# Optimization experiments

Measured on AMD Instinct MI355X. Metric: run time of the kernel, lower is better.

Reference implementation:

```python
import jax, jax.numpy as jnp
import numpy as np

DX = 1.0
DZ_MIN = 1.0
K = 3  # median filter kernel size (odd)


def median_filter3d(x):
    # x: (N, C, D, H, W); 3x3x3 windowed median with reflect padding.
    p = K // 2
    xp = jnp.pad(x, ((0, 0), (0, 0), (p, p), (p, p), (p, p)), mode='reflect')
    N, C, D, H, W = x.shape
    # 27 shifted views stacked on a new last axis (fixed small loop over kernel offsets)
    wins = jnp.stack(
        [xp[:, :, i:i + D, j:j + H, k:k + W]
         for i in range(K) for j in range(K) for k in range(K)],
        axis=-1,
    )
    # 27 elements (odd) -> torch lower-median == element at index 13 of sorted window
    return jnp.sort(wins, axis=-1)[..., (K * K * K - 1) // 2]


def setup_inputs() -> dict:
    key = jax.random.key(0)
    pred_z = jax.random.normal(key, (1, 1, 128, 192, 193), dtype=jnp.float32)
    return {"pred_z": pred_z, "iepoch": 1, "epoch_max": 100}


def reference(pred_z, iepoch, epoch_max):
    # dz along last (W) axis
    dz = pred_z[..., 1:] - pred_z[..., :-1]
    d = dz / DX
    # windowed-median smoothness loss (no NaNs in inputs -> nanmean == mean)
    smoothz = median_filter3d(d)
    loss_smooth = jnp.mean((d - smoothz) ** 2)
    # monotonicity penalty: max over clamped negative increments
    loss_mon = jnp.max(jnp.maximum(-(dz - DZ_MIN) / DX, 0.0))
    # torch.median over all elements returns sorted[(n-1)//2] (lower median)
    z0 = pred_z[..., 0].reshape(-1)
    n = z0.shape[0]
    loss_average = jnp.sort(z0)[(n - 1) // 2] ** 2
    return (loss_smooth, loss_mon, loss_average)
```

## Files before the change

### kernel.cpp

```cpp
#include <hip/hip_runtime.h>

#define NZ 128
#define NY 192
#define NXP 193
#define NX 192
#define NVOX (NZ * NY * NX)
#define NZ0 (NZ * NY)

#define TX 32
#define TY 16
#define TZ 8
#define LX 34
#define LY 18
#define LZ 10
#define LSL (LY * LX)
#define LTOT (LZ * LSL)

#define GX (NX / TX)
#define GY (NY / TY)
#define GZ (NZ / TZ)
#define NBLK (GX * GY * GZ)
#define ZB (NZ0 / 256)

__device__ double   g_ps[NBLK];
__device__ float    g_pm[NBLK];
__device__ unsigned g_hist[2048];
__device__ unsigned g_u[NZ0];

__device__ __forceinline__ int refl(int i, int n) {
    i = (i < 0) ? -i : i;
    i = (i >= n) ? (2 * n - 2 - i) : i;
    return i;
}

__device__ __forceinline__ unsigned f2sortable(float f) {
    unsigned bits = __float_as_uint(f);
    return bits ^ ((bits & 0x80000000u) ? 0xFFFFFFFFu : 0x80000000u);
}

template<int M, int N>
struct OEM {
    static __device__ __forceinline__ void run(const float* a, const float* b, float* out) {
        if constexpr (M == 0) {
#pragma unroll
            for (int i = 0; i < N; ++i) out[i] = b[i];
        } else if constexpr (N == 0) {
#pragma unroll
            for (int i = 0; i < M; ++i) out[i] = a[i];
        } else if constexpr (M == 1 && N == 1) {
            out[0] = fminf(a[0], b[0]);
            out[1] = fmaxf(a[0], b[0]);
        } else {
            constexpr int ME = (M + 1) / 2, MO = M / 2, NE = (N + 1) / 2, NO = N / 2;
            float ae[ME], be[NE];
            float ao[MO > 0 ? MO : 1], bo[NO > 0 ? NO : 1];
#pragma unroll
            for (int i = 0; i < ME; ++i) ae[i] = a[2 * i];
#pragma unroll
            for (int i = 0; i < MO; ++i) ao[i] = a[2 * i + 1];
#pragma unroll
            for (int i = 0; i < NE; ++i) be[i] = b[2 * i];
#pragma unroll
            for (int i = 0; i < NO; ++i) bo[i] = b[2 * i + 1];
            constexpr int EL = ME + NE, OL = MO + NO;
            float e[EL];
            float o[OL > 0 ? OL : 1];
            OEM<ME, NE>::run(ae, be, e);
            OEM<MO, NO>::run(ao, bo, o);
            constexpr int P = (OL < EL - 1) ? OL : (EL - 1);
            out[0] = e[0];
#pragma unroll
            for (int i = 0; i < P; ++i) {
                out[2 * i + 1] = fminf(o[i], e[i + 1]);
                out[2 * i + 2] = fmaxf(o[i], e[i + 1]);
            }
            if constexpr (EL == OL)           out[M + N - 1] = o[OL - 1];
            else if constexpr (EL == OL + 2)  out[M + N - 1] = e[EL - 1];
        }
    }
};

template<int N>
struct OES {
    static __device__ __forceinline__ void run(const float* in, float* out) {
        if constexpr (N == 1) {
            out[0] = in[0];
        } else {
            constexpr int H = N / 2;
            float s1[H], s2[N - H];
            OES<H>::run(in, s1);
            OES<N - H>::run(in + H, s2);
            OEM<H, N - H>::run(s1, s2, out);
        }
    }
};

__device__ __forceinline__ float sel27(const float* A, const float* M) {
    float t0 = fmaxf(A[0], M[12]);
    float t1 = fmaxf(A[1], M[11]);
    float t2 = fmaxf(A[2], M[10]);
    float t3 = fmaxf(A[3], M[9]);
    float t4 = fmaxf(A[4], M[8]);
    float t5 = fmaxf(A[5], M[7]);
    float t6 = fmaxf(A[6], M[6]);
    float t7 = fmaxf(A[7], M[5]);
    float t8 = fmaxf(A[8], M[4]);
    float r0 = fminf(fminf(t0, t1), fminf(t2, t3));
    float r1 = fminf(fminf(t4, t5), fminf(t6, t7));
    return fminf(fminf(r0, r1), fminf(t8, M[13]));
}

__global__ __launch_bounds__(256, 3) void fused_main(const float* __restrict__ P) {
    __shared__ float dt[LTOT];
    const int tid = threadIdx.x;
    const int bid = blockIdx.x;

    if (bid < ZB) {
        unsigned* h = (unsigned*)dt;
        for (int j = tid; j < 2048; j += 256) h[j] = 0u;
        __syncthreads();
        const int i = bid * 256 + tid;
        unsigned u = f2sortable(P[(size_t)i * NXP]);
        g_u[i] = u;
        atomicAdd(&h[u >> 21], 1u);
        __syncthreads();
        for (int j = tid; j < 2048; j += 256) {
            unsigned c = h[j];
            if (c) atomicAdd(&g_hist[j], c);
        }
        return;
    }

    const int bf = bid - ZB;
    const int bx = bf % GX;
    const int brem = bf / GX;
    const int by = brem % GY;
    const int bz = brem / GY;
    const int x0 = bx * TX, y0 = by * TY, z0t = bz * TZ;

    int goff[3], lp[3];
#pragma unroll
    for (int k = 0; k < 3; ++k) {
        int p = tid + 256 * k;
        lp[k] = (p < LSL) ? p : -1;
        if (p < LSL) {
            int xx = p % LX, yy = p / LX;
            int gy = refl(y0 + yy - 1, NY);
            int gx = refl(x0 + xx - 1, NX);
            goff[k] = gy * NXP + gx;
        }
    }
    for (int zz = 0; zz < LZ; ++zz) {
        int gz = refl(z0t + zz - 1, NZ);
        const float* __restrict__ pl = P + (size_t)gz * (NY * NXP);
#pragma unroll
        for (int k = 0; k < 3; ++k) {
            if (lp[k] >= 0) {
                float a = pl[goff[k]];
                float b = pl[goff[k] + 1];
                dt[zz * LSL + lp[k]] = b - a;
            }
        }
    }
    __syncthreads();

    const int x = tid & 31;
    const int y = tid >> 5;
    const int lbA = y * LX + x;
    const int lbB = lbA + 8 * LX;

    auto rd9 = [&](int base, float* v) {
#pragma unroll
        for (int dy = 0; dy < 3; ++dy)
#pragma unroll
            for (int dxx = 0; dxx < 3; ++dxx)
                v[dy * 3 + dxx] = dt[base + dy * LX + dxx];
    };

    float SA0[9], SA1[9], SA2[9], SB0[9], SB1[9], SB2[9];
    float cA, cB, s_acc = 0.0f, m_acc = 0.0f;

    {
        float a9[9], b9[9];
        rd9(lbA, a9);            rd9(lbB, b9);
        OES<9>::run(a9, SA0);    OES<9>::run(b9, SB0);
        rd9(lbA + LSL, a9);      rd9(lbB + LSL, b9);
        cA = a9[4];              cB = b9[4];
        OES<9>::run(a9, SA1);    OES<9>::run(b9, SB1);
    }

    auto pairstep = [&](float (&XA)[9], float (&YA)[9], float (&ZA)[9],
                        float (&XB)[9], float (&YB)[9], float (&ZB_)[9], int t) {
        float a9[9], b9[9], MA[18], MB[18];
        rd9(lbA + (t + 2) * LSL, a9);
        rd9(lbB + (t + 2) * LSL, b9);
        float cnA = a9[4], cnB = b9[4];
        OES<9>::run(a9, ZA);            OES<9>::run(b9, ZB_);
        OEM<9, 9>::run(YA, ZA, MA);     OEM<9, 9>::run(YB, ZB_, MB);
        float medA = sel27(XA, MA), medB = sel27(XB, MB);
        float dA = cA - medA, dB = cB - medB;
        s_acc = fmaf(dA, dA, fmaf(dB, dB, s_acc));
        m_acc = fmaxf(m_acc, fmaxf(1.0f - cA, 1.0f - cB));
        cA = cnA; cB = cnB;
        rd9(lbA + (t + 3) * LSL, a9);
        rd9(lbB + (t + 3) * LSL, b9);
        cnA = a9[4]; cnB = b9[4];
        OES<9>::run(a9, XA);            OES<9>::run(b9, XB);
        medA = sel27(XA, MA);           medB = sel27(XB, MB);
        dA = cA - medA; dB = cB - medB;
        s_acc = fmaf(dA, dA, fmaf(dB, dB, s_acc));
        m_acc = fmaxf(m_acc, fmaxf(1.0f - cA, 1.0f - cB));
        cA = cnA; cB = cnB;
    };

    pairstep(SA0, SA1, SA2, SB0, SB1, SB2, 0);
    pairstep(SA2, SA0, SA1, SB2, SB0, SB1, 2);
    pairstep(SA1, SA2, SA0, SB1, SB2, SB0, 4);
    pairstep(SA0, SA1, SA2, SB0, SB1, SB2, 6);

#pragma unroll
    for (int off = 32; off > 0; off >>= 1) {
        s_acc += __shfl_down(s_acc, off);
        m_acc = fmaxf(m_acc, __shfl_down(m_acc, off));
    }
    __shared__ float ss[4], sm[4];
    const int lane = tid & 63, wid = tid >> 6;
    if (lane == 0) { ss[wid] = s_acc; sm[wid] = m_acc; }
    __syncthreads();
    if (tid == 0) {
        float S = (ss[0] + ss[1]) + (ss[2] + ss[3]);
        float M = fmaxf(fmaxf(sm[0], sm[1]), fmaxf(sm[2], sm[3]));
        g_ps[bf] = (double)S;
        g_pm[bf] = M;
    }
}

__global__ __launch_bounds__(1024) void final_k(float* __restrict__ out) {
    __shared__ unsigned cand[2048];
    __shared__ unsigned s_cnt, s_med, s_b, s_r;
    __shared__ unsigned wsum[16], woff[16];
    const int tid = threadIdx.x;
    const int lane = tid & 63, wid = tid >> 6;
    const unsigned kk = (NZ0 - 1) / 2;

    unsigned h0 = g_hist[2 * tid], h1 = g_hist[2 * tid + 1];
    {
        unsigned mysum = h0 + h1, inc = mysum;
#pragma unroll
        for (int d = 1; d < 64; d <<= 1) { unsigned t2 = __shfl_up(inc, d); if (lane >= d) inc += t2; }
        if (lane == 63) wsum[wid] = inc;
        __syncthreads();
        if (tid == 0) { unsigned a = 0; for (int w = 0; w < 16; ++w) { woff[w] = a; a += wsum[w]; } }
        __syncthreads();
        unsigned exc = woff[wid] + inc - mysum;
        if (exc <= kk && kk < exc + h0) { s_b = 2u * tid; s_r = kk - exc; }
        exc += h0;
        if (exc <= kk && kk < exc + h1) { s_b = 2u * tid + 1u; s_r = kk - exc; }
    }
    __syncthreads();
    const unsigned b1 = s_b, k1 = s_r;
    g_hist[2 * tid] = 0u; g_hist[2 * tid + 1] = 0u;

    if (tid == 0) s_cnt = 0u;
    __syncthreads();
    for (int i = tid; i < NZ0; i += 1024) {
        unsigned u = g_u[i];
        if ((u >> 21) == b1) {
            unsigned idx = atomicAdd(&s_cnt, 1u);
            if (idx < 2048u) cand[idx] = u;
        }
    }
    __syncthreads();
    const unsigned m = s_cnt;

    if (m <= 2048u) {
        for (int i = tid; i < (int)m; i += 1024) {
            unsigned c = cand[i], less = 0u, eq = 0u;
            for (unsigned j = 0; j < m; ++j) {
                unsigned v = cand[j];
                less += (v < c); eq += (v == c);
            }
            if (less <= k1 && k1 < less + eq) s_med = c;
        }
        __syncthreads();
    } else {
        unsigned pref = b1, kx = k1;
        for (int j = tid; j < 2048; j += 1024) cand[j] = 0u;
        __syncthreads();
        for (int i = tid; i < NZ0; i += 1024) {
            unsigned u = g_u[i];
            if ((u >> 21) == pref) atomicAdd(&cand[(u >> 10) & 2047u], 1u);
        }
        __syncthreads();
        {
            unsigned c0 = cand[tid * 2], c1 = cand[tid * 2 + 1];
            unsigned mysum = c0 + c1, inc = mysum;
#pragma unroll
            for (int d = 1; d < 64; d <<= 1) { unsigned t2 = __shfl_up(inc, d); if (lane >= d) inc += t2; }
            if (lane == 63) wsum[wid] = inc;
            __syncthreads();
            if (tid == 0) { unsigned a = 0; for (int w = 0; w < 16; ++w) { woff[w] = a; a += wsum[w]; } }
            __syncthreads();
            unsigned exc = woff[wid] + inc - mysum;
            if (exc <= kx && kx < exc + c0) { s_b = tid * 2u; s_r = kx - exc; }
            exc += c0;
            if (exc <= kx && kx < exc + c1) { s_b = tid * 2u + 1u; s_r = kx - exc; }
        }
        __syncthreads();
        pref = (pref << 11) | s_b; kx = s_r;
        __syncthreads();
        for (int j = tid; j < 1024; j += 1024) cand[j] = 0u;
        __syncthreads();
        for (int i = tid; i < NZ0; i += 1024) {
            unsigned u = g_u[i];
            if ((u >> 10) == pref) atomicAdd(&cand[u & 1023u], 1u);
        }
        __syncthreads();
        {
            unsigned c0 = cand[tid], mysum = c0, inc = mysum;
#pragma unroll
            for (int d = 1; d < 64; d <<= 1) { unsigned t2 = __shfl_up(inc, d); if (lane >= d) inc += t2; }
            if (lane == 63) wsum[wid] = inc;
            __syncthreads();
            if (tid == 0) { unsigned a = 0; for (int w = 0; w < 16; ++w) { woff[w] = a; a += wsum[w]; } }
            __syncthreads();
            unsigned exc = woff[wid] + inc - mysum;
            if (exc <= kx && kx < exc + c0) s_b = (unsigned)tid;
        }
        __syncthreads();
        if (tid == 0) s_med = (pref << 10) | s_b;
        __syncthreads();
    }

    double s = 0.0; float mm = 0.0f;
    if (tid < NBLK) { s = g_ps[tid]; mm = g_pm[tid]; }
    if (tid < NBLK - 1024) { s += g_ps[1024 + tid]; mm = fmaxf(mm, g_pm[1024 + tid]); }
#pragma unroll
    for (int off = 32; off > 0; off >>= 1) {
        s += __shfl_down(s, off);
        mm = fmaxf(mm, __shfl_down(mm, off));
    }
    __shared__ double sd[16];
    __shared__ float sf[16];
    if (lane == 0) { sd[wid] = s; sf[wid] = mm; }
    __syncthreads();
    if (tid == 0) {
        double S = 0.0; float M = 0.0f;
        for (int w = 0; w < 16; ++w) { S += sd[w]; M = fmaxf(M, sf[w]); }
        unsigned u = s_med;
        unsigned bits = (u & 0x80000000u) ? (u ^ 0x80000000u) : ~u;
        float med = __uint_as_float(bits);
        out[0] = (float)(S / (double)NVOX);
        out[1] = M;
        out[2] = med * med;
    }
}

extern "C" void kernel_launch(void* const* d_in, const int* in_sizes, int n_in,
                              void* d_out, int out_size, void* d_ws, size_t ws_size,
                              hipStream_t stream) {
    const float* P = (const float*)d_in[0];
    float* out = (float*)d_out;

    hipLaunchKernelGGL(fused_main, dim3(ZB + NBLK), dim3(256), 0, stream, P);
    hipLaunchKernelGGL(final_k, dim3(1), dim3(1024), 0, stream, out);
}
```

Measured before the change: 104.5 us.

## Fuse final reduction into main kernel via last-block ticket

Merges the separate single-block final kernel into the main kernel. Each block takes an atomic ticket after a threadfence, and the last block to finish does the histogram median selection and the partial-sum reduction with 256 threads. This removes the second kernel launch and the gap between kernels. In exchange the tail work runs on 256 threads instead of 1024, and there is an extra atomic plus a fence in every block.

```diff
diff --git a/kernel.cpp b/kernel.cpp
--- a/kernel.cpp
+++ b/kernel.cpp
@@ -21,11 +21,13 @@
 #define GZ (NZ / TZ)
 #define NBLK (GX * GY * GZ)
 #define ZB (NZ0 / 256)
+#define NBALL (ZB + NBLK)
 
 __device__ double   g_ps[NBLK];
 __device__ float    g_pm[NBLK];
 __device__ unsigned g_hist[2048];
 __device__ unsigned g_u[NZ0];
+__device__ unsigned g_ticket;
 
 __device__ __forceinline__ int refl(int i, int n) {
     i = (i < 0) ? -i : i;
@@ -110,10 +112,17 @@
     return fminf(fminf(r0, r1), fminf(t8, M[13]));
 }
 
-__global__ __launch_bounds__(256, 3) void fused_main(const float* __restrict__ P) {
+__global__ __launch_bounds__(256, 3) void fused_all(const float* __restrict__ P,
+                                                    float* __restrict__ out) {
     __shared__ float dt[LTOT];
+    __shared__ float ss[4], sm[4];
+    __shared__ unsigned s_t, s_b, s_r, s_cnt, s_med;
+    __shared__ unsigned wsum[4], woff[4];
+    __shared__ double sd[4];
+    __shared__ float sf[4];
     const int tid = threadIdx.x;
     const int bid = blockIdx.x;
+    const int lane = tid & 63, wid = tid >> 6;
 
     if (bid < ZB) {
         unsigned* h = (unsigned*)dt;
@@ -128,156 +137,160 @@
             unsigned c = h[j];
             if (c) atomicAdd(&g_hist[j], c);
         }
-        return;
-    }
-
-    const int bf = bid - ZB;
-    const int bx = bf % GX;
-    const int brem = bf / GX;
-    const int by = brem % GY;
-    const int bz = brem / GY;
-    const int x0 = bx * TX, y0 = by * TY, z0t = bz * TZ;
-
-    int goff[3], lp[3];
-#pragma unroll
-    for (int k = 0; k < 3; ++k) {
-        int p = tid + 256 * k;
-        lp[k] = (p < LSL) ? p : -1;
-        if (p < LSL) {
-            int xx = p % LX, yy = p / LX;
-            int gy = refl(y0 + yy - 1, NY);
-            int gx = refl(x0 + xx - 1, NX);
-            goff[k] = gy * NXP + gx;
-        }
-    }
-    for (int zz = 0; zz < LZ; ++zz) {
-        int gz = refl(z0t + zz - 1, NZ);
-        const float* __restrict__ pl = P + (size_t)gz * (NY * NXP);
+    } else {
+        const int bf = bid - ZB;
+        const int bx = bf % GX;
+        const int brem = bf / GX;
+        const int by = brem % GY;
+        const int bz = brem / GY;
+        const int x0 = bx * TX, y0 = by * TY, z0t = bz * TZ;
+
+        int goff[3], lp[3];
 #pragma unroll
         for (int k = 0; k < 3; ++k) {
-            if (lp[k] >= 0) {
-                float a = pl[goff[k]];
-                float b = pl[goff[k] + 1];
-                dt[zz * LSL + lp[k]] = b - a;
-            }
-        }
-    }
-    __syncthreads();
-
-    const int x = tid & 31;
-    const int y = tid >> 5;
-    const int lbA = y * LX + x;
-    const int lbB = lbA + 8 * LX;
-
-    auto rd9 = [&](int base, float* v) {
-#pragma unroll
-        for (int dy = 0; dy < 3; ++dy)
-#pragma unroll
-            for (int dxx = 0; dxx < 3; ++dxx)
-                v[dy * 3 + dxx] = dt[base + dy * LX + dxx];
-    };
-
-    float SA0[9], SA1[9], SA2[9], SB0[9], SB1[9], SB2[9];
-    float cA, cB, s_acc = 0.0f, m_acc = 0.0f;
+            int p = tid + 256 * k;
+            lp[k] = (p < LSL) ? p : -1;
+            if (p < LSL) {
+                int xx = p % LX, yy = p / LX;
+                int gy = refl(y0 + yy - 1, NY);
+                int gx = refl(x0 + xx - 1, NX);
+                goff[k] = gy * NXP + gx;
+            }
+        }
+        for (int zz = 0; zz < LZ; ++zz) {
+            int gz = refl(z0t + zz - 1, NZ);
+            const float* __restrict__ pl = P + (size_t)gz * (NY * NXP);
+#pragma unroll
+            for (int k = 0; k < 3; ++k) {
+                if (lp[k] >= 0) {
+                    float a = pl[goff[k]];
+                    float b = pl[goff[k] + 1];
+                    dt[zz * LSL + lp[k]] = b - a;
+                }
+            }
+        }
+        __syncthreads();
+
+        const int x = tid & 31;
+        const int y = tid >> 5;
+        const int lbA = y * LX + x;
+        const int lbB = lbA + 8 * LX;
+
+        auto rd9 = [&](int base, float* v) {
+#pragma unroll
+            for (int dy = 0; dy < 3; ++dy)
+#pragma unroll
+                for (int dxx = 0; dxx < 3; ++dxx)
+                    v[dy * 3 + dxx] = dt[base + dy * LX + dxx];
+        };
+
+        float SA0[9], SA1[9], SA2[9], SB0[9], SB1[9], SB2[9];
+        float cA, cB, s_acc = 0.0f, m_acc = 0.0f;
+
+        {
+            float a9[9], b9[9];
+            rd9(lbA, a9);            rd9(lbB, b9);
+            OES<9>::run(a9, SA0);    OES<9>::run(b9, SB0);
+            rd9(lbA + LSL, a9);      rd9(lbB + LSL, b9);
+            cA = a9[4];              cB = b9[4];
+            OES<9>::run(a9, SA1);    OES<9>::run(b9, SB1);
+        }
+
+        auto pairstep = [&](float (&XA)[9], float (&YA)[9], float (&ZA)[9],
+                            float (&XB)[9], float (&YB)[9], float (&ZB_)[9], int t) {
+            float a9[9], b9[9], MA[18], MB[18];
+            rd9(lbA + (t + 2) * LSL, a9);
+            rd9(lbB + (t + 2) * LSL, b9);
+            float cnA = a9[4], cnB = b9[4];
+            OES<9>::run(a9, ZA);            OES<9>::run(b9, ZB_);
+            OEM<9, 9>::run(YA, ZA, MA);     OEM<9, 9>::run(YB, ZB_, MB);
+            float medA = sel27(XA, MA), medB = sel27(XB, MB);
+            float dA = cA - medA, dB = cB - medB;
+            s_acc = fmaf(dA, dA, fmaf(dB, dB, s_acc));
+            m_acc = fmaxf(m_acc, fmaxf(1.0f - cA, 1.0f - cB));
+            cA = cnA; cB = cnB;
+            rd9(lbA + (t + 3) * LSL, a9);
+            rd9(lbB + (t + 3) * LSL, b9);
+            cnA = a9[4]; cnB = b9[4];
+            OES<9>::run(a9, XA);            OES<9>::run(b9, XB);
+            medA = sel27(XA, MA);           medB = sel27(XB, MB);
+            dA = cA - medA; dB = cB - medB;
+            s_acc = fmaf(dA, dA, fmaf(dB, dB, s_acc));
+            m_acc = fmaxf(m_acc, fmaxf(1.0f - cA, 1.0f - cB));
+            cA = cnA; cB = cnB;
+        };
+
+        pairstep(SA0, SA1, SA2, SB0, SB1, SB2, 0);
+        pairstep(SA2, SA0, SA1, SB2, SB0, SB1, 2);
+        pairstep(SA1, SA2, SA0, SB1, SB2, SB0, 4);
+        pairstep(SA0, SA1, SA2, SB0, SB1, SB2, 6);
+
+#pragma unroll
+        for (int off = 32; off > 0; off >>= 1) {
+            s_acc += __shfl_down(s_acc, off);
+            m_acc = fmaxf(m_acc, __shfl_down(m_acc, off));
+        }
+        if (lane == 0) { ss[wid] = s_acc; sm[wid] = m_acc; }
+        __syncthreads();
+        if (tid == 0) {
+            float S = (ss[0] + ss[1]) + (ss[2] + ss[3]);
+            float M = fmaxf(fmaxf(sm[0], sm[1]), fmaxf(sm[2], sm[3]));
+            g_ps[bf] = (double)S;
+            g_pm[bf] = M;
+        }
+    }
+
+    __threadfence();
+    __syncthreads();
+    if (tid == 0) s_t = atomicAdd(&g_ticket, 1u);
+    __syncthreads();
+    if (s_t != (unsigned)(NBALL - 1)) return;
+
+    __threadfence();
+    unsigned* sc = (unsigned*)dt;
+    const unsigned kk = (NZ0 - 1) / 2;
 
     {
-        float a9[9], b9[9];
-        rd9(lbA, a9);            rd9(lbB, b9);
-        OES<9>::run(a9, SA0);    OES<9>::run(b9, SB0);
-        rd9(lbA + LSL, a9);      rd9(lbB + LSL, b9);
-        cA = a9[4];              cB = b9[4];
-        OES<9>::run(a9, SA1);    OES<9>::run(b9, SB1);
-    }
-
-    auto pairstep = [&](float (&XA)[9], float (&YA)[9], float (&ZA)[9],
-                        float (&XB)[9], float (&YB)[9], float (&ZB_)[9], int t) {
-        float a9[9], b9[9], MA[18], MB[18];
-        rd9(lbA + (t + 2) * LSL, a9);
-        rd9(lbB + (t + 2) * LSL, b9);
-        float cnA = a9[4], cnB = b9[4];
-        OES<9>::run(a9, ZA);            OES<9>::run(b9, ZB_);
-        OEM<9, 9>::run(YA, ZA, MA);     OEM<9, 9>::run(YB, ZB_, MB);
-        float medA = sel27(XA, MA), medB = sel27(XB, MB);
-        float dA = cA - medA, dB = cB - medB;
-        s_acc = fmaf(dA, dA, fmaf(dB, dB, s_acc));
-        m_acc = fmaxf(m_acc, fmaxf(1.0f - cA, 1.0f - cB));
-        cA = cnA; cB = cnB;
-        rd9(lbA + (t + 3) * LSL, a9);
-        rd9(lbB + (t + 3) * LSL, b9);
-        cnA = a9[4]; cnB = b9[4];
-        OES<9>::run(a9, XA);            OES<9>::run(b9, XB);
-        medA = sel27(XA, MA);           medB = sel27(XB, MB);
-        dA = cA - medA; dB = cB - medB;
-        s_acc = fmaf(dA, dA, fmaf(dB, dB, s_acc));
-        m_acc = fmaxf(m_acc, fmaxf(1.0f - cA, 1.0f - cB));
-        cA = cnA; cB = cnB;
-    };
-
-    pairstep(SA0, SA1, SA2, SB0, SB1, SB2, 0);
-    pairstep(SA2, SA0, SA1, SB2, SB0, SB1, 2);
-    pairstep(SA1, SA2, SA0, SB1, SB2, SB0, 4);
-    pairstep(SA0, SA1, SA2, SB0, SB1, SB2, 6);
-
-#pragma unroll
-    for (int off = 32; off > 0; off >>= 1) {
-        s_acc += __shfl_down(s_acc, off);
-        m_acc = fmaxf(m_acc, __shfl_down(m_acc, off));
-    }
-    __shared__ float ss[4], sm[4];
-    const int lane = tid & 63, wid = tid >> 6;
-    if (lane == 0) { ss[wid] = s_acc; sm[wid] = m_acc; }
-    __syncthreads();
-    if (tid == 0) {
-        float S = (ss[0] + ss[1]) + (ss[2] + ss[3]);
-        float M = fmaxf(fmaxf(sm[0], sm[1]), fmaxf(sm[2], sm[3]));
-        g_ps[bf] = (double)S;
-        g_pm[bf] = M;
-    }
-}
-
-__global__ __launch_bounds__(1024) void final_k(float* __restrict__ out) {
-    __shared__ unsigned cand[2048];
-    __shared__ unsigned s_cnt, s_med, s_b, s_r;
-    __shared__ unsigned wsum[16], woff[16];
-    const int tid = threadIdx.x;
-    const int lane = tid & 63, wid = tid >> 6;
-    const unsigned kk = (NZ0 - 1) / 2;
-
-    unsigned h0 = g_hist[2 * tid], h1 = g_hist[2 * tid + 1];
-    {
-        unsigned mysum = h0 + h1, inc = mysum;
+        unsigned my[8], mysum = 0u;
+#pragma unroll
+        for (int j = 0; j < 8; ++j) { my[j] = g_hist[tid * 8 + j]; mysum += my[j]; }
+#pragma unroll
+        for (int j = 0; j < 8; ++j) g_hist[tid * 8 + j] = 0u;
+        unsigned inc = mysum;
 #pragma unroll
         for (int d = 1; d < 64; d <<= 1) { unsigned t2 = __shfl_up(inc, d); if (lane >= d) inc += t2; }
         if (lane == 63) wsum[wid] = inc;
         __syncthreads();
-        if (tid == 0) { unsigned a = 0; for (int w = 0; w < 16; ++w) { woff[w] = a; a += wsum[w]; } }
+        if (tid == 0) { unsigned a = 0; for (int w = 0; w < 4; ++w) { woff[w] = a; a += wsum[w]; } }
         __syncthreads();
         unsigned exc = woff[wid] + inc - mysum;
-        if (exc <= kk && kk < exc + h0) { s_b = 2u * tid; s_r = kk - exc; }
-        exc += h0;
-        if (exc <= kk && kk < exc + h1) { s_b = 2u * tid + 1u; s_r = kk - exc; }
+#pragma unroll
+        for (int j = 0; j < 8; ++j) {
+            unsigned c = my[j];
+            if (exc <= kk && kk < exc + c) { s_b = (unsigned)(tid * 8 + j); s_r = kk - exc; }
+            exc += c;
+        }
     }
     __syncthreads();
     const unsigned b1 = s_b, k1 = s_r;
-    g_hist[2 * tid] = 0u; g_hist[2 * tid + 1] = 0u;
 
     if (tid == 0) s_cnt = 0u;
     __syncthreads();
-    for (int i = tid; i < NZ0; i += 1024) {
+    for (int i = tid; i < NZ0; i += 256) {
         unsigned u = g_u[i];
         if ((u >> 21) == b1) {
             unsigned idx = atomicAdd(&s_cnt, 1u);
-            if (idx < 2048u) cand[idx] = u;
+            if (idx < 2048u) sc[idx] = u;
         }
     }
     __syncthreads();
     const unsigned m = s_cnt;
 
     if (m <= 2048u) {
-        for (int i = tid; i < (int)m; i += 1024) {
-            unsigned c = cand[i], less = 0u, eq = 0u;
+        for (int i = tid; i < (int)m; i += 256) {
+            unsigned c = sc[i], less = 0u, eq = 0u;
             for (unsigned j = 0; j < m; ++j) {
-                unsigned v = cand[j];
+                unsigned v = sc[j];
                 less += (v < c); eq += (v == c);
             }
             if (less <= k1 && k1 < less + eq) s_med = c;
@@ -285,47 +298,61 @@
         __syncthreads();
     } else {
         unsigned pref = b1, kx = k1;
-        for (int j = tid; j < 2048; j += 1024) cand[j] = 0u;
-        __syncthreads();
-        for (int i = tid; i < NZ0; i += 1024) {
+        __syncthreads();
+        for (int j = tid; j < 2048; j += 256) sc[j] = 0u;
+        __syncthreads();
+        for (int i = tid; i < NZ0; i += 256) {
             unsigned u = g_u[i];
-            if ((u >> 21) == pref) atomicAdd(&cand[(u >> 10) & 2047u], 1u);
+            if ((u >> 21) == pref) atomicAdd(&sc[(u >> 10) & 2047u], 1u);
         }
         __syncthreads();
         {
-            unsigned c0 = cand[tid * 2], c1 = cand[tid * 2 + 1];
-            unsigned mysum = c0 + c1, inc = mysum;
+            unsigned my[8], mysum = 0u;
+#pragma unroll
+            for (int j = 0; j < 8; ++j) { my[j] = sc[tid * 8 + j]; mysum += my[j]; }
+            unsigned inc = mysum;
 #pragma unroll
             for (int d = 1; d < 64; d <<= 1) { unsigned t2 = __shfl_up(inc, d); if (lane >= d) inc += t2; }
             if (lane == 63) wsum[wid] = inc;
             __syncthreads();
-            if (tid == 0) { unsigned a = 0; for (int w = 0; w < 16; ++w) { woff[w] = a; a += wsum[w]; } }
+            if (tid == 0) { unsigned a = 0; for (int w = 0; w < 4; ++w) { woff[w] = a; a += wsum[w]; } }
             __syncthreads();
             unsigned exc = woff[wid] + inc - mysum;
-            if (exc <= kx && kx < exc + c0) { s_b = tid * 2u; s_r = kx - exc; }
-            exc += c0;
-            if (exc <= kx && kx < exc + c1) { s_b = tid * 2u + 1u; s_r = kx - exc; }
+#pragma unroll
+            for (int j = 0; j < 8; ++j) {
+                unsigned c = my[j];
+                if (exc <= kx && kx < exc + c) { s_b = (unsigned)(tid * 8 + j); s_r = kx - exc; }
+                exc += c;
+            }
         }
         __syncthreads();
         pref = (pref << 11) | s_b; kx = s_r;
         __syncthreads();
-        for (int j = tid; j < 1024; j += 1024) cand[j] = 0u;
-        __syncthreads();
-        for (int i = tid; i < NZ0; i += 1024) {
+        for (int j = tid; j < 1024; j += 256) sc[j] = 0u;
+        __syncthreads();
+        for (int i = tid; i < NZ0; i += 256) {
             unsigned u = g_u[i];
-            if ((u >> 10) == pref) atomicAdd(&cand[u & 1023u], 1u);
+            if ((u >> 10) == pref) atomicAdd(&sc[u & 1023u], 1u);
         }
         __syncthreads();
         {
-            unsigned c0 = cand[tid], mysum = c0, inc = mysum;
+            unsigned my[4], mysum = 0u;
+#pragma unroll
+            for (int j = 0; j < 4; ++j) { my[j] = sc[tid * 4 + j]; mysum += my[j]; }
+            unsigned inc = mysum;
 #pragma unroll
             for (int d = 1; d < 64; d <<= 1) { unsigned t2 = __shfl_up(inc, d); if (lane >= d) inc += t2; }
             if (lane == 63) wsum[wid] = inc;
             __syncthreads();
-            if (tid == 0) { unsigned a = 0; for (int w = 0; w < 16; ++w) { woff[w] = a; a += wsum[w]; } }
+            if (tid == 0) { unsigned a = 0; for (int w = 0; w < 4; ++w) { woff[w] = a; a += wsum[w]; } }
             __syncthreads();
             unsigned exc = woff[wid] + inc - mysum;
-            if (exc <= kx && kx < exc + c0) s_b = (unsigned)tid;
+#pragma unroll
+            for (int j = 0; j < 4; ++j) {
+                unsigned c = my[j];
+                if (exc <= kx && kx < exc + c) s_b = (unsigned)(tid * 4 + j);
+                exc += c;
+            }
         }
         __syncthreads();
         if (tid == 0) s_med = (pref << 10) | s_b;
@@ -333,26 +360,27 @@
     }
 
     double s = 0.0; float mm = 0.0f;
-    if (tid < NBLK) { s = g_ps[tid]; mm = g_pm[tid]; }
-    if (tid < NBLK - 1024) { s += g_ps[1024 + tid]; mm = fmaxf(mm, g_pm[1024 + tid]); }
+    for (int i = tid; i < NBLK; i += 256) {
+        s += g_ps[i];
+        mm = fmaxf(mm, g_pm[i]);
+    }
 #pragma unroll
     for (int off = 32; off > 0; off >>= 1) {
         s += __shfl_down(s, off);
         mm = fmaxf(mm, __shfl_down(mm, off));
     }
-    __shared__ double sd[16];
-    __shared__ float sf[16];
     if (lane == 0) { sd[wid] = s; sf[wid] = mm; }
     __syncthreads();
     if (tid == 0) {
-        double S = 0.0; float M = 0.0f;
-        for (int w = 0; w < 16; ++w) { S += sd[w]; M = fmaxf(M, sf[w]); }
+        double S = (sd[0] + sd[1]) + (sd[2] + sd[3]);
+        float M = fmaxf(fmaxf(sf[0], sf[1]), fmaxf(sf[2], sf[3]));
         unsigned u = s_med;
         unsigned bits = (u & 0x80000000u) ? (u ^ 0x80000000u) : ~u;
         float med = __uint_as_float(bits);
         out[0] = (float)(S / (double)NVOX);
         out[1] = M;
         out[2] = med * med;
+        g_ticket = 0u;
     }
 }
 
@@ -361,7 +389,5 @@
                               hipStream_t stream) {
     const float* P = (const float*)d_in[0];
     float* out = (float*)d_out;
-
-    hipLaunchKernelGGL(fused_main, dim3(ZB + NBLK), dim3(256), 0, stream, P);
-    hipLaunchKernelGGL(final_k, dim3(1), dim3(1024), 0, stream, out);
-}
+    hipLaunchKernelGGL(fused_all, dim3(NBALL), dim3(256), 0, stream, P, out);
+}
```

After: 190.2 us. 1.82x slower.
